# Performance work log

Measured on AMD Instinct MI355X. Metric: run time of the kernel, lower is better.

Reference implementation:

```python
import jax, jax.numpy as jnp
import numpy as np

N = 10000      # nodes
E = 50000      # edges
NS = 48        # multiplicity of 0e (scalars)
NV = 10        # multiplicity of 1o (vectors)
NEF = 128      # n_edge_features
HID = 128      # hidden_features
W1N = NS * NS  # path 0e x 0e -> 0e
W2N = NS * NV  # path 0e x 1o -> 1o
W3N = NV * NV  # path 1o x 0e -> 1o
W4N = NV * NS  # path 1o x 1o -> 0e
WTOT = W1N + W2N + W3N + W4N  # tp.weight_numel = 3364
EPS = 1e-5
INV_SQRT3 = float(1.0 / np.sqrt(3.0))   # w3j(1,1,0) coefficient
NORM0 = float(1.0 / np.sqrt(NS + NV))   # path normalization into 0e output
NORM1 = float(1.0 / np.sqrt(NS + NV))   # path normalization into 1o output


def setup_inputs() -> dict:
    key = jax.random.key(0)
    ks = jax.random.split(key, 6)
    node_attr = jax.random.normal(ks[0], (N, NS + 3 * NV), jnp.float32)
    edge_index = jax.random.randint(ks[1], (2, E), 0, N, dtype=jnp.int32)
    edge_attr = jax.random.normal(ks[2], (E, NEF), jnp.float32)
    edge_sh = jax.random.normal(ks[3], (E, 4), jnp.float32)
    fc_w1 = jax.random.normal(ks[4], (NEF, HID), jnp.float32) / np.sqrt(NEF)
    fc_b1 = jnp.zeros((HID,), jnp.float32)
    fc_w2 = jax.random.normal(ks[5], (HID, WTOT), jnp.float32) / np.sqrt(HID)
    fc_b2 = jnp.zeros((WTOT,), jnp.float32)
    bn_weight = jnp.ones((NS + NV,), jnp.float32)  # affine scale per irrep
    bn_bias = jnp.zeros((NS,), jnp.float32)        # bias only for scalars
    return {"node_attr": node_attr, "edge_index": edge_index,
            "edge_attr": edge_attr, "edge_sh": edge_sh,
            "fc_w1": fc_w1, "fc_b1": fc_b1, "fc_w2": fc_w2, "fc_b2": fc_b2,
            "bn_weight": bn_weight, "bn_bias": bn_bias}


def reference(node_attr, edge_index, edge_attr, edge_sh,
              fc_w1, fc_b1, fc_w2, fc_b2, bn_weight, bn_bias):
    edge_src, edge_dst = edge_index[0], edge_index[1]

    # gather node features per edge
    x = node_attr[edge_dst]                       # [E, 78]
    s_in = x[:, :NS]                              # [E, NS] scalars (0e)
    v_in = x[:, NS:].reshape(E, NV, 3)            # [E, NV, 3] vectors (1o)
    sh0 = edge_sh[:, 0:1]                         # [E, 1]   sh 0e
    sh1 = edge_sh[:, 1:4]                         # [E, 3]   sh 1o

    # weight-generating MLP (per-edge tensor-product weights)
    h = jax.nn.relu(edge_attr @ fc_w1 + fc_b1)
    w = h @ fc_w2 + fc_b2                         # [E, 3364]
    w1 = w[:, :W1N].reshape(E, NS, NS)
    w2 = w[:, W1N:W1N + W2N].reshape(E, NS, NV)
    w3 = w[:, W1N + W2N:W1N + W2N + W3N].reshape(E, NV, NV)
    w4 = w[:, W1N + W2N + W3N:].reshape(E, NV, NS)

    # Clebsch-Gordan tensor product (4 paths)
    dot = jnp.einsum('evi,ei->ev', v_in, sh1) * INV_SQRT3      # 1o x 1o -> 0e
    out0 = (jnp.einsum('euv,eu->ev', w1, s_in) * sh0
            + jnp.einsum('euv,eu->ev', w4, dot)) * NORM0        # [E, NS]
    out1 = (jnp.einsum('euv,eu->ev', w2, s_in)[:, :, None] * sh1[:, None, :]
            + jnp.einsum('euv,eui->evi', w3, v_in) * sh0[:, :, None]) * NORM1  # [E, NV, 3]
    tp = jnp.concatenate([out0, out1.reshape(E, 3 * NV)], axis=-1)  # [E, 78]

    # scatter-mean to nodes
    summed = jax.ops.segment_sum(tp, edge_src, num_segments=N)
    cnt = jax.ops.segment_sum(jnp.ones((E,), tp.dtype), edge_src, num_segments=N)
    out = summed / jnp.maximum(cnt, 1.0)[:, None]

    # residual (in/out dims equal, so F.pad is a no-op)
    out = out + node_attr

    # e3nn-style equivariant BatchNorm (training mode, component normalization)
    s = out[:, :NS]
    v = out[:, NS:].reshape(N, NV, 3)
    s = s - s.mean(axis=0)
    s = s * jax.lax.rsqrt((s ** 2).mean(axis=0) + EPS) * bn_weight[:NS] + bn_bias
    vn = (v ** 2).mean(axis=-1).mean(axis=0)       # [NV] mean squared component
    v = v * (jax.lax.rsqrt(vn + EPS) * bn_weight[NS:])[None, :, None]
    return jnp.concatenate([s, v.reshape(N, 3 * NV)], axis=-1)
```

## Files before the change

kernel.cpp:

```cpp
#include <hip/hip_runtime.h>
#include <hip/hip_bf16.h>

#define NS 48
#define NV 10
#define NATT 78
#define HID 128
#define WTOT 3364
#define NEDGE 50000
#define NNODE 10000
#define EPAD 50048
#define EPSV 1e-5f
#define INV_SQRT3 0.57735026918962576f
#define NORM0 0.13130643285972254f
#define NORM1 0.13130643285972254f

#define FXS  2147483648.0f
#define FXSI (1.0 / 2147483648.0)
#define FXQ  268435456.0f
#define FXQI (1.0 / 268435456.0)

#define CPAD2 3744
#define NTILE 232
#define NGRP  78

#define NBLK_NODE 256

using half8 = __attribute__((ext_vector_type(8))) _Float16;
using f32x4 = __attribute__((ext_vector_type(4))) float;

__device__ __forceinline__ unsigned short f2h(float x) {
  union { _Float16 h; unsigned short u; } v;
  v.h = (_Float16)x;
  return v.u;
}

__device__ __forceinline__ void atomFx(unsigned long long* p, float x) {
  long long q = (long long)rintf(x * FXS);
  atomicAdd(p, (unsigned long long)q);
}

__device__ __forceinline__ int cp_to_src(int cp) {
  if (cp < 2304) return cp;
  if (cp < 2784) return 2884 + (cp - 2304);
  if (cp < 3552) { int t = cp - 2784; int u = t >> 4, v = t & 15;
                   return (v < 10) ? (2304 + u * 10 + v) : -1; }
  if (cp < 3712) { int t = cp - 3552; int u = t >> 4, v = t & 15;
                   return (v < 10) ? (2784 + u * 10 + v) : -1; }
  return -1;
}

__global__ __launch_bounds__(256) void k_prep_bt2(const float* __restrict__ w2,
                                                  unsigned short* __restrict__ Bt2) {
  int idx = blockIdx.x * 256 + threadIdx.x;
  int cp = idx >> 7, k = idx & 127;
  int c_src = cp_to_src(cp);
  Bt2[idx] = (c_src >= 0) ? f2h(w2[(size_t)k * WTOT + c_src]) : (unsigned short)0;
}

__global__ __launch_bounds__(256) void k_fc1(const float* __restrict__ ea,
                                             const float* __restrict__ w1,
                                             const float* __restrict__ b1,
                                             unsigned short* __restrict__ hbf) {
  __shared__ float sT[128][36];
  int tid = threadIdx.x;
  int e0 = blockIdx.x * 32;
  for (int i = tid; i < 32 * 128; i += 256) {
    int el = i >> 7, k = i & 127;
    int e = e0 + el;
    sT[k][el] = (e < NEDGE) ? ea[(size_t)e * 128 + k] : 0.f;
  }
  __syncthreads();
  int cg = tid & 31;
  int eg = tid >> 5;
  float acc[4][4] = {};
  #pragma unroll 4
  for (int k = 0; k < 128; ++k) {
    float4 a = *(const float4*)&sT[k][eg * 4];
    float4 w = *(const float4*)&w1[k * 128 + cg * 4];
    float av[4] = {a.x, a.y, a.z, a.w};
    float wv[4] = {w.x, w.y, w.z, w.w};
    #pragma unroll
    for (int ii = 0; ii < 4; ++ii)
      #pragma unroll
      for (int jj = 0; jj < 4; ++jj)
        acc[ii][jj] += av[ii] * wv[jj];
  }
  float bb[4];
  #pragma unroll
  for (int jj = 0; jj < 4; ++jj) bb[jj] = b1[cg * 4 + jj];
  #pragma unroll
  for (int ii = 0; ii < 4; ++ii) {
    int e = e0 + eg * 4 + ii;
    bool val = e < NEDGE;
    unsigned short h4[4];
    #pragma unroll
    for (int jj = 0; jj < 4; ++jj) {
      float r = val ? fmaxf(acc[ii][jj] + bb[jj], 0.f) : 0.f;
      h4[jj] = f2h(r);
    }
    uint2 pk;
    pk.x = (unsigned)h4[0] | ((unsigned)h4[1] << 16);
    pk.y = (unsigned)h4[2] | ((unsigned)h4[3] << 16);
    *(uint2*)(hbf + (size_t)e * 128 + cg * 4) = pk;
  }
}

__global__ __launch_bounds__(256, 3) void k_tp(const unsigned short* __restrict__ hbf,
                                               const unsigned short* __restrict__ Bt2,
                                               const float* __restrict__ fb2,
                                               const int* __restrict__ eidx,
                                               const float* __restrict__ node_attr,
                                               const float* __restrict__ esh,
                                               unsigned long long* __restrict__ summed,
                                               unsigned* __restrict__ cnt) {
  __shared__ half8    bufB[1536];
  __shared__ float    sFT[48][64];
  __shared__ float    vFL[64][30];
  __shared__ _Float16 b2pH[CPAD2];
  __shared__ float    p0FL[64], q0FL[64];
  __shared__ float    sh1nL[64][3];
  __shared__ int      srcL[64], dstL[64];

  const int tid  = threadIdx.x;
  const int wid  = tid >> 6;
  const int lane = tid & 63;
  const int col  = lane & 15;
  const int quad = lane >> 4;
  const int e0   = blockIdx.x * 64;
  const int elb  = wid * 16 + quad * 4;

  if (tid < 64) {
    int eg = e0 + tid;
    bool val = eg < NEDGE;
    srcL[tid] = val ? eidx[eg] : -1;
    dstL[tid] = val ? eidx[NEDGE + eg] : -1;
    float sh0 = 0.f, s1x = 0.f, s1y = 0.f, s1z = 0.f;
    if (val) {
      float4 s4 = *(const float4*)&esh[(size_t)eg * 4];
      sh0 = s4.x; s1x = s4.y; s1y = s4.z; s1z = s4.w;
    }
    p0FL[tid] = sh0 * NORM0;
    q0FL[tid] = sh0 * NORM1;
    sh1nL[tid][0] = s1x * NORM1; sh1nL[tid][1] = s1y * NORM1; sh1nL[tid][2] = s1z * NORM1;
  }
  for (int i = tid; i < CPAD2; i += 256) {
    int c_src = cp_to_src(i);
    b2pH[i] = (c_src >= 0) ? (_Float16)fb2[c_src] : (_Float16)0.f;
  }
  __syncthreads();
  for (int i = tid; i < 64 * NATT; i += 256) {
    int el = i / NATT, a = i % NATT;
    int dst = dstL[el];
    float x = (dst >= 0) ? node_attr[(size_t)dst * NATT + a] : 0.f;
    if (a < NS) sFT[a][el] = x; else vFL[el][a - NS] = x;
  }
  __syncthreads();

  half8 aF0, aF1, aF2, aF3;
  {
    const half8* hp = (const half8*)hbf;
    size_t arow = (size_t)(e0 + wid * 16 + col) * 16;
    aF0 = hp[arow + 0 * 4 + quad];
    aF1 = hp[arow + 1 * 4 + quad];
    aF2 = hp[arow + 2 * 4 + quad];
    aF3 = hp[arow + 3 * 4 + quad];
  }
  float p0v[4];
  #pragma unroll
  for (int r = 0; r < 4; ++r) p0v[r] = p0FL[elb + r];

  const char* bt2c = (const char*)Bt2;
  const int colS = tid >> 4, k8sS = tid & 15;
  const size_t gOff = (size_t)(colS * 16 + (k8sS ^ colS)) * 16;

  #define STAGE3(G) do {                                                           \
    int _t0 = (G) * 3;                                                             \
    char* _db = (char*)bufB + ((G) & 1) * 12288 + wid * 1024;                      \
    _Pragma("unroll")                                                              \
    for (int _t = 0; _t < 3; ++_t)                                                 \
      __builtin_amdgcn_global_load_lds(                                            \
        (const __attribute__((address_space(1))) void*)(bt2c + (size_t)(_t0 + _t) * 4096 + gOff), \
        (__attribute__((address_space(3))) void*)(_db + _t * 4096), 16, 0, 0);     \
  } while (0)

  STAGE3(0); STAGE3(1);

  float acc0[4][3] = {};
  float t1a[4] = {};
  float t3a[4][3] = {};

  const int k0 = (0 * 4 + quad) ^ col;
  const int k1 = (1 * 4 + quad) ^ col;
  const int k2 = (2 * 4 + quad) ^ col;
  const int k3 = (3 * 4 + quad) ^ col;
  const int cb = col * 16;

  #pragma unroll 1
  for (int p = 0; p < NGRP; ++p) {
    asm volatile("s_waitcnt vmcnt(0)\n\ts_barrier" ::: "memory");

    const int bb = ((p & 1) << 9) + ((p & 1) << 8) + cb;
    half8 b00 = bufB[bb +   0 + k0], b01 = bufB[bb +   0 + k1],
          b02 = bufB[bb +   0 + k2], b03 = bufB[bb +   0 + k3];
    half8 b10 = bufB[bb + 256 + k0], b11 = bufB[bb + 256 + k1],
          b12 = bufB[bb + 256 + k2], b13 = bufB[bb + 256 + k3];
    half8 b20 = bufB[bb + 512 + k0], b21 = bufB[bb + 512 + k1],
          b22 = bufB[bb + 512 + k2], b23 = bufB[bb + 512 + k3];

    __builtin_amdgcn_s_setprio(1);
    f32x4 m0 = {0.f, 0.f, 0.f, 0.f};
    f32x4 m1 = {0.f, 0.f, 0.f, 0.f};
    f32x4 m2 = {0.f, 0.f, 0.f, 0.f};
    m0 = __builtin_amdgcn_mfma_f32_16x16x32_f16(aF0, b00, m0, 0, 0, 0);
    m1 = __builtin_amdgcn_mfma_f32_16x16x32_f16(aF0, b10, m1, 0, 0, 0);
    m2 = __builtin_amdgcn_mfma_f32_16x16x32_f16(aF0, b20, m2, 0, 0, 0);
    m0 = __builtin_amdgcn_mfma_f32_16x16x32_f16(aF1, b01, m0, 0, 0, 0);
    m1 = __builtin_amdgcn_mfma_f32_16x16x32_f16(aF1, b11, m1, 0, 0, 0);
    m2 = __builtin_amdgcn_mfma_f32_16x16x32_f16(aF1, b21, m2, 0, 0, 0);
    m0 = __builtin_amdgcn_mfma_f32_16x16x32_f16(aF2, b02, m0, 0, 0, 0);
    m1 = __builtin_amdgcn_mfma_f32_16x16x32_f16(aF2, b12, m1, 0, 0, 0);
    m2 = __builtin_amdgcn_mfma_f32_16x16x32_f16(aF2, b22, m2, 0, 0, 0);
    m0 = __builtin_amdgcn_mfma_f32_16x16x32_f16(aF3, b03, m0, 0, 0, 0);
    m1 = __builtin_amdgcn_mfma_f32_16x16x32_f16(aF3, b13, m1, 0, 0, 0);
    m2 = __builtin_amdgcn_mfma_f32_16x16x32_f16(aF3, b23, m2, 0, 0, 0);
    __builtin_amdgcn_s_setprio(0);

    asm volatile("s_waitcnt lgkmcnt(0)\n\ts_barrier" ::: "memory");
    if (p < NGRP - 2) STAGE3(p + 2);

    float b2c0 = (float)b2pH[(p * 3 + 0) * 16 + col];
    float b2c1 = (float)b2pH[(p * 3 + 1) * 16 + col];
    float b2c2 = (float)b2pH[(p * 3 + 2) * 16 + col];
    if (p < 48) {
      #pragma unroll
      for (int r = 0; r < 4; ++r) {
        float sfac = sFT[p][elb + r] * p0v[r];
        acc0[r][0] += (m0[r] + b2c0) * sfac;
        acc0[r][1] += (m1[r] + b2c1) * sfac;
        acc0[r][2] += (m2[r] + b2c2) * sfac;
      }
    } else if (p < 58) {
      int u3 = (p - 48) * 3;
      #pragma unroll
      for (int r = 0; r < 4; ++r) {
        int el = elb + r;
        float dfac = (vFL[el][u3]     * sh1nL[el][0] +
                      vFL[el][u3 + 1] * sh1nL[el][1] +
                      vFL[el][u3 + 2] * sh1nL[el][2]) * INV_SQRT3;
        acc0[r][0] += (m0[r] + b2c0) * dfac;
        acc0[r][1] += (m1[r] + b2c1) * dfac;
        acc0[r][2] += (m2[r] + b2c2) * dfac;
      }
    } else if (p < 74) {
      int u0 = (p - 58) * 3;
      #pragma unroll
      for (int r = 0; r < 4; ++r) {
        int el = elb + r;
        t1a[r] += (m0[r] + b2c0) * sFT[u0][el]
                + (m1[r] + b2c1) * sFT[u0 + 1][el]
                + (m2[r] + b2c2) * sFT[u0 + 2][el];
      }
    } else {
      int ub = (p - 74) * 3;
      int T0 = p * 3;
      #pragma unroll
      for (int r = 0; r < 4; ++r) {
        int el = elb + r;
        {
          float w = m0[r] + b2c0;
          t3a[r][0] += w * vFL[el][(ub + 0) * 3 + 0];
          t3a[r][1] += w * vFL[el][(ub + 0) * 3 + 1];
          t3a[r][2] += w * vFL[el][(ub + 0) * 3 + 2];
        }
        if (T0 + 1 < NTILE) {
          float w = m1[r] + b2c1;
          t3a[r][0] += w * vFL[el][(ub + 1) * 3 + 0];
          t3a[r][1] += w * vFL[el][(ub + 1) * 3 + 1];
          t3a[r][2] += w * vFL[el][(ub + 1) * 3 + 2];
        }
        if (T0 + 2 < NTILE) {
          float w = m2[r] + b2c2;
          t3a[r][0] += w * vFL[el][(ub + 2) * 3 + 0];
          t3a[r][1] += w * vFL[el][(ub + 2) * 3 + 1];
          t3a[r][2] += w * vFL[el][(ub + 2) * 3 + 2];
        }
      }
    }
  }
  #undef STAGE3

  #pragma unroll
  for (int r = 0; r < 4; ++r) {
    int el = elb + r;
    int src = srcL[el];
    if (src < 0) continue;
    unsigned long long* dp = &summed[(size_t)src * NATT];
    #pragma unroll
    for (int j = 0; j < 3; ++j)
      atomFx(dp + j * 16 + col, acc0[r][j]);
    if (col < 10) {
      float q0 = q0FL[el];
      #pragma unroll
      for (int i = 0; i < 3; ++i)
        atomFx(dp + NS + col * 3 + i,
               t1a[r] * sh1nL[el][i] + t3a[r][i] * q0);
    }
  }
  if (tid < 64 && srcL[tid] >= 0) atomicAdd(&cnt[srcL[tid]], 1u);
}

__global__ __launch_bounds__(256) void k_node(const unsigned long long* __restrict__ summed,
                                              const unsigned* __restrict__ cnt,
                                              const float* __restrict__ node_attr,
                                              float* __restrict__ outp,
                                              unsigned long long* __restrict__ partials) {
  __shared__ unsigned long long ls[NS], lq[NS], lv[NV];
  int tid = threadIdx.x;
  if (tid < NS) { ls[tid] = 0ull; lq[tid] = 0ull; }
  if (tid < NV) lv[tid] = 0ull;
  __syncthreads();
  for (int i = blockIdx.x * 256 + tid; i < NNODE * NATT; i += NBLK_NODE * 256) {
    int row = i / NATT, colc = i % NATT;
    long long sv = (long long)summed[i];
    float sum = (float)((double)sv * FXSI);
    float x = sum / fmaxf((float)cnt[row], 1.f) + node_attr[i];
    outp[i] = x;
    if (colc < NS) {
      atomicAdd(&ls[colc], (unsigned long long)(long long)rintf(x * FXS));
      atomicAdd(&lq[colc], (unsigned long long)(long long)rintf(x * x * FXQ));
    } else {
      atomicAdd(&lv[(colc - NS) / 3], (unsigned long long)(long long)rintf(x * x * FXQ));
    }
  }
  __syncthreads();
  if (tid < 128) {
    unsigned long long v = 0ull;
    if (tid < NS)            v = ls[tid];
    else if (tid < 2 * NS)   v = lq[tid - NS];
    else if (tid < 96 + NV)  v = lv[tid - 96];
    partials[(size_t)blockIdx.x * 128 + tid] = v;
  }
}

__global__ __launch_bounds__(128) void k_stats(const unsigned long long* __restrict__ partials,
                                               unsigned long long* __restrict__ stats) {
  int c = threadIdx.x;
  unsigned long long s = 0ull;
  for (int b = 0; b < NBLK_NODE; ++b) s += partials[(size_t)b * 128 + c];
  stats[c] = s;
}

__global__ __launch_bounds__(256) void k_bn(const float* __restrict__ outp,
                                            const unsigned long long* __restrict__ stats,
                                            const float* __restrict__ bnw,
                                            const float* __restrict__ bnb,
                                            float* __restrict__ out) {
  int i = blockIdx.x * 256 + threadIdx.x;
  if (i >= NNODE * NATT) return;
  int colc = i % NATT;
  float x = outp[i];
  float r;
  if (colc < NS) {
    float mean = (float)((double)(long long)stats[colc] * (FXSI / NNODE));
    float ex2  = (float)((double)(long long)stats[NS + colc] * (FXQI / NNODE));
    float var  = ex2 - mean * mean;
    r = (x - mean) * rsqrtf(var + EPSV) * bnw[colc] + bnb[colc];
  } else {
    int u = (colc - NS) / 3;
    float vn = (float)((double)(long long)stats[96 + u] * (FXQI / (3.0 * NNODE)));
    r = x * rsqrtf(vn + EPSV) * bnw[NS + u];
  }
  out[i] = r;
}

extern "C" void kernel_launch(void* const* d_in, const int* in_sizes, int n_in,
                              void* d_out, int out_size, void* d_ws, size_t ws_size,
                              hipStream_t stream) {
  const float* node_attr = (const float*)d_in[0];
  const int*   eidx      = (const int*)d_in[1];
  const float* edge_attr = (const float*)d_in[2];
  const float* esh       = (const float*)d_in[3];
  const float* fw1       = (const float*)d_in[4];
  const float* fb1       = (const float*)d_in[5];
  const float* fw2       = (const float*)d_in[6];
  const float* fb2       = (const float*)d_in[7];
  const float* bnw       = (const float*)d_in[8];
  const float* bnb       = (const float*)d_in[9];
  float* out = (float*)d_out;

  char* ws = (char*)d_ws;
  unsigned short*     Bt2      = (unsigned short*)(ws + 0);
  unsigned short*     hbf      = (unsigned short*)(ws + 958464);
  unsigned long long* summed   = (unsigned long long*)(ws + 13770752);
  unsigned*           cnt      = (unsigned*)(ws + 20010752);
  float*              outp     = (float*)(ws + 0);
  unsigned long long* partials = (unsigned long long*)(ws + 3120000);
  unsigned long long* stats    = (unsigned long long*)(ws + 3382144);

  hipMemsetAsync(ws + 13770752, 0, 6240000 + 40000, stream);

  k_prep_bt2<<<(CPAD2 * 128) / 256, 256, 0, stream>>>(fw2, Bt2);
  k_fc1<<<EPAD / 32, 256, 0, stream>>>(edge_attr, fw1, fb1, hbf);
  k_tp<<<EPAD / 64, 256, 0, stream>>>(hbf, Bt2, fb2, eidx, node_attr, esh, summed, cnt);
  k_node<<<NBLK_NODE, 256, 0, stream>>>(summed, cnt, node_attr, outp, partials);
  k_stats<<<1, 128, 0, stream>>>(partials, stats);
  int nelem_blocks = (NNODE * NATT + 255) / 256;
  k_bn<<<nelem_blocks, 256, 0, stream>>>(outp, stats, bnw, bnb, out);
}
```

Measured before the change: 318.9 us.

## Fuse weight prep, FC1 and memset into one kernel using fp16 MFMA for FC1

```diff
diff --git a/kernel.cpp b/kernel.cpp
--- a/kernel.cpp
+++ b/kernel.cpp
@@ -25,6 +25,11 @@
 
 #define NBLK_NODE 256
 
+#define PREP_BLKS 1872
+#define FC1_BLKS  782
+#define ZERO_BYTES 6280000
+#define ZERO_BLKS 1534
+
 using half8 = __attribute__((ext_vector_type(8))) _Float16;
 using f32x4 = __attribute__((ext_vector_type(4))) float;
 
@@ -49,59 +54,68 @@
   return -1;
 }
 
-__global__ __launch_bounds__(256) void k_prep_bt2(const float* __restrict__ w2,
-                                                  unsigned short* __restrict__ Bt2) {
-  int idx = blockIdx.x * 256 + threadIdx.x;
-  int cp = idx >> 7, k = idx & 127;
-  int c_src = cp_to_src(cp);
-  Bt2[idx] = (c_src >= 0) ? f2h(w2[(size_t)k * WTOT + c_src]) : (unsigned short)0;
-}
-
-__global__ __launch_bounds__(256) void k_fc1(const float* __restrict__ ea,
-                                             const float* __restrict__ w1,
-                                             const float* __restrict__ b1,
-                                             unsigned short* __restrict__ hbf) {
-  __shared__ float sT[128][36];
-  int tid = threadIdx.x;
-  int e0 = blockIdx.x * 32;
-  for (int i = tid; i < 32 * 128; i += 256) {
-    int el = i >> 7, k = i & 127;
-    int e = e0 + el;
-    sT[k][el] = (e < NEDGE) ? ea[(size_t)e * 128 + k] : 0.f;
+__global__ __launch_bounds__(256) void k_front(const float* __restrict__ w2,
+                                               unsigned short* __restrict__ Bt2,
+                                               const float* __restrict__ ea,
+                                               const float* __restrict__ w1,
+                                               const float* __restrict__ b1,
+                                               unsigned short* __restrict__ hbf,
+                                               char* __restrict__ zbase) {
+  __shared__ _Float16 w1T[128][136];
+  const int bid = blockIdx.x;
+  const int tid = threadIdx.x;
+
+  if (bid < PREP_BLKS) {
+    int idx = bid * 256 + tid;
+    int cp = idx >> 7, k = idx & 127;
+    int c_src = cp_to_src(cp);
+    Bt2[idx] = (c_src >= 0) ? f2h(w2[(size_t)k * WTOT + c_src]) : (unsigned short)0;
+    return;
+  }
+  if (bid >= PREP_BLKS + FC1_BLKS) {
+    size_t off = ((size_t)(bid - PREP_BLKS - FC1_BLKS) * 256 + tid) * 16;
+    if (off < ZERO_BYTES) *(uint4*)(zbase + off) = make_uint4(0, 0, 0, 0);
+    return;
+  }
+
+  const int b  = bid - PREP_BLKS;
+  const int e0 = b * 64;
+  for (int i = tid; i < 128 * 128; i += 256) {
+    int k = i >> 7, n = i & 127;
+    w1T[n][k] = (_Float16)w1[i];
   }
   __syncthreads();
-  int cg = tid & 31;
-  int eg = tid >> 5;
-  float acc[4][4] = {};
-  #pragma unroll 4
-  for (int k = 0; k < 128; ++k) {
-    float4 a = *(const float4*)&sT[k][eg * 4];
-    float4 w = *(const float4*)&w1[k * 128 + cg * 4];
-    float av[4] = {a.x, a.y, a.z, a.w};
-    float wv[4] = {w.x, w.y, w.z, w.w};
+
+  const int lane = tid & 63, wid = tid >> 6;
+  const int col = lane & 15, quad = lane >> 4;
+  int e  = e0 + wid * 16 + col;
+  int er = (e < NEDGE) ? e : 0;
+  const float* ear = ea + (size_t)er * 128;
+  half8 aF[4];
+  #pragma unroll
+  for (int ks = 0; ks < 4; ++ks) {
+    float4 x0 = *(const float4*)&ear[ks * 32 + quad * 8];
+    float4 x1 = *(const float4*)&ear[ks * 32 + quad * 8 + 4];
+    half8 a;
+    a[0] = (_Float16)x0.x; a[1] = (_Float16)x0.y; a[2] = (_Float16)x0.z; a[3] = (_Float16)x0.w;
+    a[4] = (_Float16)x1.x; a[5] = (_Float16)x1.y; a[6] = (_Float16)x1.z; a[7] = (_Float16)x1.w;
+    aF[ks] = a;
+  }
+  const int erow = e0 + wid * 16 + quad * 4;
+  #pragma unroll
+  for (int t = 0; t < 8; ++t) {
+    float b1c = b1[t * 16 + col];
+    f32x4 m = {0.f, 0.f, 0.f, 0.f};
     #pragma unroll
-    for (int ii = 0; ii < 4; ++ii)
-      #pragma unroll
-      for (int jj = 0; jj < 4; ++jj)
-        acc[ii][jj] += av[ii] * wv[jj];
-  }
-  float bb[4];
-  #pragma unroll
-  for (int jj = 0; jj < 4; ++jj) bb[jj] = b1[cg * 4 + jj];
-  #pragma unroll
-  for (int ii = 0; ii < 4; ++ii) {
-    int e = e0 + eg * 4 + ii;
-    bool val = e < NEDGE;
-    unsigned short h4[4];
+    for (int ks = 0; ks < 4; ++ks) {
+      half8 bf = *(const half8*)&w1T[t * 16 + col][ks * 32 + quad * 8];
+      m = __builtin_amdgcn_mfma_f32_16x16x32_f16(aF[ks], bf, m, 0, 0, 0);
+    }
     #pragma unroll
-    for (int jj = 0; jj < 4; ++jj) {
-      float r = val ? fmaxf(acc[ii][jj] + bb[jj], 0.f) : 0.f;
-      h4[jj] = f2h(r);
-    }
-    uint2 pk;
-    pk.x = (unsigned)h4[0] | ((unsigned)h4[1] << 16);
-    pk.y = (unsigned)h4[2] | ((unsigned)h4[3] << 16);
-    *(uint2*)(hbf + (size_t)e * 128 + cg * 4) = pk;
+    for (int r = 0; r < 4; ++r) {
+      float h = fmaxf(m[r] + b1c, 0.f);
+      hbf[(size_t)(erow + r) * 128 + t * 16 + col] = f2h(h);
+    }
   }
 }
 
@@ -397,10 +411,8 @@
   unsigned long long* partials = (unsigned long long*)(ws + 3120000);
   unsigned long long* stats    = (unsigned long long*)(ws + 3382144);
 
-  hipMemsetAsync(ws + 13770752, 0, 6240000 + 40000, stream);
-
-  k_prep_bt2<<<(CPAD2 * 128) / 256, 256, 0, stream>>>(fw2, Bt2);
-  k_fc1<<<EPAD / 32, 256, 0, stream>>>(edge_attr, fw1, fb1, hbf);
+  k_front<<<PREP_BLKS + FC1_BLKS + ZERO_BLKS, 256, 0, stream>>>(
+      fw2, Bt2, edge_attr, fw1, fb1, hbf, ws + 13770752);
   k_tp<<<EPAD / 64, 256, 0, stream>>>(hbf, Bt2, fb2, eidx, node_attr, esh, summed, cnt);
   k_node<<<NBLK_NODE, 256, 0, stream>>>(summed, cnt, node_attr, outp, partials);
   k_stats<<<1, 128, 0, stream>>>(partials, stats);
```

Result: faster. 293.8 us (-7.9%).
